# Kernel optimization log

Hardware: AMD Instinct MI355X
Metric: run time of the kernel (lower is better)

The kernel has to match this reference:

```python
import jax, jax.numpy as jnp
import numpy as np

V, N, F, H, E, C = 3, 20000, 256, 256, 160000, 32
NH = 8  # transformer heads


def setup_inputs() -> dict:
    key = jax.random.key(0)
    ks = jax.random.split(key, 24)
    r = lambda i, shape, s=0.05: jax.random.normal(ks[i], shape, jnp.float32) * s
    ri = lambda i, shape: jax.random.randint(ks[i], shape, 0, N)
    loop = jnp.arange(N)
    return {
        "x": r(0, (V, N, F), 1.0),
        "edge_src": ri(1, (V, E)),
        "edge_dst": ri(2, (V, E)),
        "g_src": jnp.concatenate([ri(3, (E,)), loop]),
        "g_dst": jnp.concatenate([ri(4, (E,)), loop]),
        "rand_w": r(5, (N, 1), 1.0),
        "gcn_W": r(6, (V, F, H)), "gcn_b": jnp.zeros((V, H)),
        "gat_W": r(7, (V, H, H)), "gat_asrc": r(8, (V, H)),
        "gat_adst": r(9, (V, H)), "gat_b": jnp.zeros((V, H)),
        "enc_Wqkv": r(10, (2, 3 * H, H)), "enc_bqkv": jnp.zeros((2, 3 * H)),
        "enc_Wo": r(11, (2, H, H)), "enc_bo": jnp.zeros((2, H)),
        "enc_W1": r(12, (2, 4 * H, H)), "enc_b1": jnp.zeros((2, 4 * H)),
        "enc_W2": r(13, (2, H, 4 * H)), "enc_b2": jnp.zeros((2, H)),
        "enc_ln1g": jnp.ones((2, H)), "enc_ln1b": jnp.zeros((2, H)),
        "enc_ln2g": jnp.ones((2, H)), "enc_ln2b": jnp.zeros((2, H)),
        "att_P": r(14, (2, H, 128)), "att_Pb": jnp.zeros((2, 128)),
        "att_q": r(15, (2, 128)),
        "mg_fc": r(16, (H, C)), "mg_al": r(17, (C,)), "mg_ar": r(18, (C,)),
        "mg_res": r(19, (H, C)),
    }


def _ln(x, g, b, eps=1e-5):
    m = x.mean(-1, keepdims=True)
    v = ((x - m) ** 2).mean(-1, keepdims=True)
    return (x - m) * jax.lax.rsqrt(v + eps) * g + b


def _gcn(x, src, dst, W, b):
    # PyG GCNConv: add self-loops, symmetric normalization, linear, scatter-sum
    n = x.shape[0]
    loop = jnp.arange(n)
    s = jnp.concatenate([src, loop])
    d = jnp.concatenate([dst, loop])
    h = x @ W  # [n, H]
    deg = jax.ops.segment_sum(jnp.ones_like(d, x.dtype), d, num_segments=n)
    dinv = jnp.where(deg > 0, jax.lax.rsqrt(deg), 0.0)
    norm = dinv[s] * dinv[d]  # [E+n]
    return jax.ops.segment_sum(h[s] * norm[:, None], d, num_segments=n) + b


def _edge_softmax(e, dst, n):
    m = jax.ops.segment_max(e, dst, num_segments=n)
    ee = jnp.exp(e - m[dst])
    z = jax.ops.segment_sum(ee, dst, num_segments=n)
    return ee / z[dst]


def _gat(x, src, dst, W, a_src, a_dst, b, slope=0.2):
    # PyG GATConv, heads=1, eval mode: add self-loops, attention softmax per dst
    n = x.shape[0]
    loop = jnp.arange(n)
    s = jnp.concatenate([src, loop])
    d = jnp.concatenate([dst, loop])
    h = x @ W
    e = jax.nn.leaky_relu((h @ a_src)[s] + (h @ a_dst)[d], slope)
    alpha = _edge_softmax(e, d, n)
    return jax.ops.segment_sum(h[s] * alpha[:, None], d, num_segments=n) + b


def _enc(x, Wqkv, bqkv, Wo, bo, W1, b1, W2, b2, g1, be1, g2, be2):
    # nn.TransformerEncoderLayer (post-norm, relu, eval): x is [S=V, B=N, H]
    S, B, Hd = x.shape
    dh = Hd // NH
    qkv = x @ Wqkv.T + bqkv
    q, k, v = jnp.split(qkv, 3, axis=-1)
    q = q.reshape(S, B, NH, dh)
    k = k.reshape(S, B, NH, dh)
    v = v.reshape(S, B, NH, dh)
    sc = jnp.einsum('sbhd,tbhd->bhst', q, k) * (1.0 / np.sqrt(dh))
    o = jnp.einsum('bhst,tbhd->sbhd', jax.nn.softmax(sc, axis=-1), v)
    o = o.reshape(S, B, Hd) @ Wo.T + bo
    h1 = _ln(x + o, g1, be1)
    ff = jax.nn.relu(h1 @ W1.T + b1) @ W2.T + b2
    return _ln(h1 + ff, g2, be2)


def reference(x, edge_src, edge_dst, g_src, g_dst, rand_w,
              gcn_W, gcn_b, gat_W, gat_asrc, gat_adst, gat_b,
              enc_Wqkv, enc_bqkv, enc_Wo, enc_bo, enc_W1, enc_b1, enc_W2, enc_b2,
              enc_ln1g, enc_ln1b, enc_ln2g, enc_ln2b,
              att_P, att_Pb, att_q, mg_fc, mg_al, mg_ar, mg_res):
    # multi-view GCN + relu
    emb1 = jax.nn.relu(jax.vmap(_gcn)(x, edge_src, edge_dst, gcn_W, gcn_b))
    a0 = _enc(emb1, enc_Wqkv[0], enc_bqkv[0], enc_Wo[0], enc_bo[0],
              enc_W1[0], enc_b1[0], enc_W2[0], enc_b2[0],
              enc_ln1g[0], enc_ln1b[0], enc_ln2g[0], enc_ln2b[0])
    # multi-view GAT + relu
    emb2 = jax.nn.relu(jax.vmap(_gat, in_axes=(0, 0, 0, 0, 0, 0, 0))(
        a0, edge_src, edge_dst, gat_W, gat_asrc, gat_adst, gat_b))
    a1 = _enc(emb2, enc_Wqkv[1], enc_bqkv[1], enc_Wo[1], enc_bo[1],
              enc_W1[1], enc_b1[1], enc_W2[1], enc_b2[1],
              enc_ln1g[1], enc_ln1b[1], enc_ln2g[1], enc_ln2b[1])
    # Attention over views (dim 0): tanh branch and relu branch, random blend
    w0 = jnp.tanh(a1 @ att_P[0] + att_Pb[0]) @ att_q[0][:, None]  # [V, N, 1]
    x1 = (jax.nn.softmax(w0, axis=0) * a1).sum(0)
    w1 = jax.nn.relu(a1 @ att_P[1] + att_Pb[1]) @ att_q[1][:, None]
    x2 = (jax.nn.softmax(w1, axis=0) * a1).sum(0)
    aw = jax.nn.softmax(rand_w, axis=0)  # [N, 1]
    g = aw * x1 + (1.0 - aw) * x2  # global_emb [N, H]
    # myGATConv (DGL-style, 1 head, residual linear, no bias/activation)
    f = g @ mg_fc  # [N, C]
    e = jax.nn.leaky_relu((f @ mg_al)[g_src] + (f @ mg_ar)[g_dst], 0.2)
    alpha = _edge_softmax(e, g_dst, N)
    rst = jax.ops.segment_sum(f[g_src] * alpha[:, None], g_dst, num_segments=N)
    rst = rst + g @ mg_res
    nrm = jnp.linalg.norm(rst, axis=1, keepdims=True)
    logits = rst / jnp.maximum(nrm, 1e-12)
    return (a0, a1, logits, g)
```

## Files before the change

### kernel.cpp

```cpp
#include <hip/hip_runtime.h>
#include <hip/hip_bf16.h>
#include <math.h>

namespace {
constexpr int kV  = 3;
constexpr int kN  = 20000;
constexpr int kF  = 256;
constexpr int kH  = 256;
constexpr int kE  = 160000;
constexpr int kC  = 32;
constexpr int kNH = 8;
constexpr int kSN = kV * kN;
constexpr int kE2 = kE + kN;
constexpr int kMP = 60160;

constexpr size_t OFF_T1   = 0;
constexpr size_t OFF_T2   = OFF_T1 + (size_t)kMP * 256;
constexpr size_t OFF_T3   = OFF_T2 + (size_t)kMP * 256;
constexpr size_t OFF_BIGB = OFF_T3 + (size_t)kMP * 256;
constexpr size_t OFF_SB   = OFF_BIGB + (size_t)kMP * 512;
constexpr size_t OFF_AB   = OFF_SB + (size_t)kMP * 128;
constexpr size_t OFF_WB   = OFF_AB + (size_t)kMP * 128;
constexpr size_t OFF_GWB  = OFF_WB + 786432;
constexpr size_t OFF_PB   = OFF_GWB + 196608;
constexpr size_t OFF_DEG  = OFF_PB + 32768;
constexpr size_t OFF_EL   = OFF_DEG + (size_t)kV * kN;
constexpr size_t OFF_ER   = OFF_EL  + (size_t)kV * kN;
constexpr size_t OFF_W0   = OFF_ER  + (size_t)kV * kN;
constexpr size_t OFF_W1   = OFF_W0  + (size_t)kV * kN;
constexpr size_t OFF_FB   = OFF_W1  + (size_t)kV * kN;
constexpr size_t OFF_R2   = OFF_FB  + (size_t)kN * kC;
constexpr size_t OFF_RST  = OFF_R2  + (size_t)kN * kC;
constexpr size_t OFF_EL2  = OFF_RST + (size_t)kN * kC;
constexpr size_t OFF_ER2  = OFF_EL2 + kN;
constexpr size_t OFF_ST   = OFF_ER2 + kN;
constexpr size_t OFF_INT  = OFF_ST + 4;
constexpr size_t ICNT  = 0;
constexpr size_t ICNT2 = ICNT  + (size_t)kV * kN;
constexpr size_t IOFF  = ICNT2 + kN;
constexpr size_t IOFF2 = IOFF  + (size_t)kV * kN;
constexpr size_t ICUR  = IOFF2 + kN;
constexpr size_t ICUR2 = ICUR  + (size_t)kV * kN;
constexpr size_t ICSR  = ICUR2 + kN;
constexpr size_t ICSR2 = ICSR  + (size_t)kV * kE;
}

typedef __attribute__((ext_vector_type(4))) float f32x4;
typedef __attribute__((ext_vector_type(8))) __bf16 bf16x8;

__device__ __forceinline__ float lrelu(float x) { return x > 0.f ? x : 0.2f * x; }
__device__ __forceinline__ unsigned short f2b(float f) {
    unsigned u = __float_as_uint(f);
    return (unsigned short)((u + 0x7FFFu + ((u >> 16) & 1u)) >> 16);
}
__device__ __forceinline__ float b2f(unsigned short h) {
    return __uint_as_float((unsigned)h << 16);
}
__device__ __forceinline__ float fast_tanh(float x) {
    float xc = fminf(fmaxf(x, -15.f), 15.f);
    float e = __expf(2.0f * xc);
    return (e - 1.0f) / (e + 1.0f);
}


__global__ void cvt_k(const float* __restrict__ in, unsigned short* __restrict__ out, int n4) {
    int i = blockIdx.x * 256 + threadIdx.x;
    if (i >= n4) return;
    float4 v = reinterpret_cast<const float4*>(in)[i];
    ushort4 o;
    o.x = f2b(v.x); o.y = f2b(v.y); o.z = f2b(v.z); o.w = f2b(v.w);
    reinterpret_cast<ushort4*>(out)[i] = o;
}

__global__ void tcvt_k(const float* __restrict__ in, unsigned short* __restrict__ out,
                       int K, int N, int total) {
    int gid = blockIdx.x * 256 + threadIdx.x;
    if (gid >= total) return;
    int per = K * N;
    int v = gid / per, r = gid - v * per;
    int n = r / K, k = r - n * K;
    out[gid] = f2b(in[(size_t)v * per + (size_t)k * N + n]);
}

template <int ACT, bool WF32, bool WB16>
__global__ __launch_bounds__(256, 4) void mgemm_k(const unsigned short* __restrict__ A,
                                                  const unsigned short* __restrict__ W,
                                                  const float* __restrict__ bias,
                                                  float* __restrict__ Cf,
                                                  unsigned short* __restrict__ Cb,
                                                  int M, int N, int K,
                                                  long zA, long zW, long zC) {
    static_assert(WF32 != WB16, "exactly one output path");
    __shared__ __align__(16) unsigned short shbuf[16384];

    const int tid  = threadIdx.x;
    const int lane = tid & 63;

    const int gx = gridDim.x;
    const int nwg = gx * gridDim.y;
    const int orig = blockIdx.y * gx + blockIdx.x;
    const int q = nwg >> 3, rr = nwg & 7;
    const int xcd = orig & 7, pos = orig >> 3;
    const int nid = (xcd < rr ? xcd * (q + 1) : rr * (q + 1) + (xcd - rr) * q) + pos;
    const int bm = (nid / gx) * 128, bn = (nid % gx) * 128;

    A += (size_t)blockIdx.z * zA;
    W += (size_t)blockIdx.z * zW;
    const size_t zrow = (size_t)blockIdx.z * zC;

    const int wv = tid >> 6;
    const int wm = (wv >> 1) * 64, wn = (wv & 1) * 64;
    const int fr = lane & 15;

    const int r0 = tid >> 2;
    const int xorv = (r0 >> 1) & 3;
// ... 45 lines not shown
        for (int mi = 0; mi < 4; ++mi)
            av[mi] = *reinterpret_cast<const bf16x8*>(As + (wm + mi * 16 + fr) * 32 + slr);
#pragma unroll
        for (int ni = 0; ni < 4; ++ni)
            bv[ni] = *reinterpret_cast<const bf16x8*>(Ws + (wn + ni * 16 + fr) * 32 + slr);
#pragma unroll
        for (int mi = 0; mi < 4; ++mi)
#pragma unroll
            for (int ni = 0; ni < 4; ++ni)
                acc[mi][ni] = __builtin_amdgcn_mfma_f32_16x16x32_bf16(av[mi], bv[ni], acc[mi][ni], 0, 0, 0);
        __syncthreads();
        cur ^= 1;
    }

    const int crow = (lane >> 4) * 4;
    const int ccol = lane & 15;

    if (WB16) {
#pragma unroll
        for (int mi = 0; mi < 4; ++mi)
#pragma unroll
            for (int r = 0; r < 4; ++r) {
                const int row = wm + mi * 16 + crow + r;
#pragma unroll
                for (int ni = 0; ni < 4; ++ni) {
                    const int col = wn + ni * 16 + ccol;
                    float v = acc[mi][ni][r];
                    if (bias) v += bias[bn + col];
                    if (ACT == 1) v = fmaxf(v, 0.f);
                    if (ACT == 2) v = fast_tanh(v);
                    if (ACT == 3) v = (bn + col < 128) ? fast_tanh(v) : fmaxf(v, 0.f);
                    shbuf[row * 128 + col] = f2b(v);
                }
            }
        __syncthreads();
#pragma unroll
        for (int it = 0; it < 8; ++it) {
            const int fl = it * 2048 + tid * 8;
            const int row = fl >> 7, col = fl & 127;
            const int grow = bm + row;
            if (grow < M) {
                uint4 d = *reinterpret_cast<const uint4*>(shbuf + row * 128 + col);
                *reinterpret_cast<uint4*>(Cb + (zrow + grow) * (size_t)N + bn + col) = d;
            }
        }
    } else {
        float* epf = reinterpret_cast<float*>(shbuf);
#pragma unroll
        for (int half = 0; half < 2; ++half) {
            if ((wm >> 6) == half) {
#pragma unroll
                for (int mi = 0; mi < 4; ++mi)
#pragma unroll
                    for (int r = 0; r < 4; ++r) {
                        const int row = mi * 16 + crow + r;
#pragma unroll
                        for (int ni = 0; ni < 4; ++ni) {
                            const int col = wn + ni * 16 + ccol;
                            float v = acc[mi][ni][r];
                            if (bias) v += bias[bn + col];
                            if (ACT == 1) v = fmaxf(v, 0.f);
                            if (ACT == 2) v = fast_tanh(v);
                            if (ACT == 3) v = (bn + col < 128) ? fast_tanh(v) : fmaxf(v, 0.f);
                            epf[row * 128 + col] = v;
                        }
                    }
            }
            __syncthreads();
#pragma unroll
            for (int it = 0; it < 8; ++it) {
                const int fl = it * 1024 + tid * 4;
                const int row = fl >> 7, col = fl & 127;
                const int grow = bm + half * 64 + row;
                if (grow < M) {
                    float4 d = *reinterpret_cast<const float4*>(epf + row * 128 + col);
                    *reinterpret_cast<float4*>(Cf + (zrow + grow) * (size_t)N + bn + col) = d;
                }
            }
            __syncthreads();
        }
    }
}

template <int ACT>
__global__ __launch_bounds__(256) void gemm_k(const float* __restrict__ A,
                                              const float* __restrict__ B,
                                              const float* __restrict__ bias,
                                              float* __restrict__ Cmat,
                                              int M, int Nn, int K) {
    __shared__ float As[16][64];
    __shared__ float Bs[16][68];
    const int tid  = threadIdx.x;
    const int bm   = blockIdx.y * 64;
    const int bn   = blockIdx.x * 64;
    const int tx   = tid & 15, ty = tid >> 4;
    const int arow = tid >> 2;
    const int acol = (tid & 3) << 2;
    const int brow = tid >> 4;
    const int bcol = (tid & 15) << 2;
    const int gm   = bm + arow;
    float acc[4][4] = {{0.f,0.f,0.f,0.f},{0.f,0.f,0.f,0.f},{0.f,0.f,0.f,0.f},{0.f,0.f,0.f,0.f}};

    for (int k0 = 0; k0 < K; k0 += 16) {
        float4 av = make_float4(0.f, 0.f, 0.f, 0.f);
        if (gm < M) av = *reinterpret_cast<const float4*>(A + (size_t)gm * K + (k0 + acol));
        As[acol + 0][arow] = av.x;
        As[acol + 1][arow] = av.y;
        As[acol + 2][arow] = av.z;
        As[acol + 3][arow] = av.w;

        const int gn = bn + bcol;
        const float* Brow = B + (size_t)(k0 + brow) * Nn;
        float4 bv;
        if (gn + 3 < Nn) {
            bv = *reinterpret_cast<const float4*>(Brow + gn);
        } else {
            bv.x = (gn + 0 < Nn) ? Brow[gn + 0] : 0.f;
            bv.y = (gn + 1 < Nn) ? Brow[gn + 1] : 0.f;
            bv.z = (gn + 2 < Nn) ? Brow[gn + 2] : 0.f;
            bv.w = (gn + 3 < Nn) ? Brow[gn + 3] : 0.f;
        }
        *reinterpret_cast<float4*>(&Bs[brow][bcol]) = bv;
        __syncthreads();

#pragma unroll
        for (int k = 0; k < 16; ++k) {
            float4 a4 = *reinterpret_cast<const float4*>(&As[k][ty << 2]);
            float4 b4 = *reinterpret_cast<const float4*>(&Bs[k][tx << 2]);
            acc[0][0] += a4.x * b4.x; acc[0][1] += a4.x * b4.y; acc[0][2] += a4.x * b4.z; acc[0][3] += a4.x * b4.w;
            acc[1][0] += a4.y * b4.x; acc[1][1] += a4.y * b4.y; acc[1][2] += a4.y * b4.z; acc[1][3] += a4.y * b4.w;
            acc[2][0] += a4.z * b4.x; acc[2][1] += a4.z * b4.y; acc[2][2] += a4.z * b4.z; acc[2][3] += a4.z * b4.w;
            acc[3][0] += a4.w * b4.x; acc[3][1] += a4.w * b4.y; acc[3][2] += a4.w * b4.z; acc[3][3] += a4.w * b4.w;
        }
        __syncthreads();
    }

#pragma unroll
    for (int i = 0; i < 4; ++i) {
        int m = bm + (ty << 2) + i;
        if (m >= M) continue;
#pragma unroll
        for (int j = 0; j < 4; ++j) {
            int n = bn + (tx << 2) + j;
            if (n >= Nn) continue;
            float v = acc[i][j];
            if (bias) v += bias[n];
            if (ACT == 1) v = fmaxf(v, 0.f);
            if (ACT == 2) v = fast_tanh(v);
            Cmat[(size_t)m * Nn + n] = v;
        }
    }
}

template <bool WF32>
__global__ __launch_bounds__(256) void ln_add_k(const unsigned short* __restrict__ x,
                                                const unsigned short* __restrict__ y,
                                                const float* __restrict__ g, const float* __restrict__ b,
                                                float* __restrict__ outf, unsigned short* __restrict__ outb,
                                                int rows) {
    int r = blockIdx.x * 4 + (threadIdx.x >> 6);
    if (r >= rows) return;
    int lane = threadIdx.x & 63;
    size_t base = (size_t)r * 256 + lane * 4;
    ushort4 xu = *reinterpret_cast<const ushort4*>(x + base);
    ushort4 yu = *reinterpret_cast<const ushort4*>(y + base);
    float4 t;
    t.x = b2f(xu.x) + b2f(yu.x); t.y = b2f(xu.y) + b2f(yu.y);
    t.z = b2f(xu.z) + b2f(yu.z); t.w = b2f(xu.w) + b2f(yu.w);
    float s = t.x + t.y + t.z + t.w;
#pragma unroll
    for (int off = 32; off > 0; off >>= 1) s += __shfl_xor(s, off, 64);
    float mean = s * (1.0f / 256.0f);
    float4 d;
    d.x = t.x - mean; d.y = t.y - mean; d.z = t.z - mean; d.w = t.w - mean;
    float s2 = d.x * d.x + d.y * d.y + d.z * d.z + d.w * d.w;
#pragma unroll
    for (int off = 32; off > 0; off >>= 1) s2 += __shfl_xor(s2, off, 64);
    float rs = rsqrtf(s2 * (1.0f / 256.0f) + 1e-5f);
    float4 gv = *reinterpret_cast<const float4*>(g + lane * 4);
    float4 bv = *reinterpret_cast<const float4*>(b + lane * 4);
    float4 o;
    o.x = d.x * rs * gv.x + bv.x;
    o.y = d.y * rs * gv.y + bv.y;
    o.z = d.z * rs * gv.z + bv.z;
    o.w = d.w * rs * gv.w + bv.w;
    if (WF32) *reinterpret_cast<float4*>(outf + base) = o;
    ushort4 ob;
    ob.x = f2b(o.x); ob.y = f2b(o.y); ob.z = f2b(o.z); ob.w = f2b(o.w);
    *reinterpret_cast<ushort4*>(outb + base) = ob;
}

__global__ void rowdot2_k(const float* __restrict__ A, const float* __restrict__ v1,
                          const float* __restrict__ v2, float* __restrict__ o1,
                          float* __restrict__ o2, int rows, int K, int rowsPerVec, int vecStride) {
    int r = blockIdx.x;
    if (r >= rows) return;
    int lane = threadIdx.x;
    const float* base = A + (size_t)r * K;
    int vo = (r / rowsPerVec) * vecStride;
    float s1 = 0.f, s2 = 0.f;
    for (int c = lane; c < K; c += 64) {
        float a = base[c];
        s1 += a * v1[vo + c];
        if (v2) s2 += a * v2[vo + c];
    }
#pragma unroll
    for (int off = 32; off > 0; off >>= 1) {
        s1 += __shfl_xor(s1, off, 64);
        s2 += __shfl_xor(s2, off, 64);
    }
    if (lane == 0) { o1[r] = s1; if (o2) o2[r] = s2; }
}

__global__ __launch_bounds__(256) void attdot_k(const unsigned short* __restrict__ A, const float* __restrict__ q,
                                                float* __restrict__ o1, float* __restrict__ o2, int rows) {
    int r = blockIdx.x * 4 + (threadIdx.x >> 6);
    if (r >= rows) return;
    int lane = threadIdx.x & 63;
    const unsigned short* row = A + (size_t)r * 256;
    ushort2 va = *reinterpret_cast<const ushort2*>(row + lane * 2);
    ushort2 vb = *reinterpret_cast<const ushort2*>(row + 128 + lane * 2);
    float2 qa = *reinterpret_cast<const float2*>(q + lane * 2);
    float2 qb = *reinterpret_cast<const float2*>(q + 128 + lane * 2);
    float s1 = b2f(va.x) * qa.x + b2f(va.y) * qa.y;
    float s2 = b2f(vb.x) * qb.x + b2f(vb.y) * qb.y;
#pragma unroll
    for (int off = 32; off > 0; off >>= 1) {
        s1 += __shfl_xor(s1, off, 64);
        s2 += __shfl_xor(s2, off, 64);
    }
    if (lane == 0) { o1[r] = s1; o2[r] = s2; }
}

__global__ void rowdot2b_k(const unsigned short* __restrict__ A, const float* __restrict__ v1,
                           const float* __restrict__ v2, float* __restrict__ o1,
                           float* __restrict__ o2, int rows, int K, int rowsPerVec, int vecStride) {
    int r = blockIdx.x;
    if (r >= rows) return;
    int lane = threadIdx.x;
    const unsigned short* base = A + (size_t)r * K;
    int vo = (r / rowsPerVec) * vecStride;
    float s1 = 0.f, s2 = 0.f;
    for (int c = lane * 4; c < K; c += 256) {
        ushort4 a4 = *reinterpret_cast<const ushort4*>(base + c);
        float4 w1 = *reinterpret_cast<const float4*>(v1 + vo + c);
        float4 w2 = *reinterpret_cast<const float4*>(v2 + vo + c);
        s1 += b2f(a4.x) * w1.x + b2f(a4.y) * w1.y + b2f(a4.z) * w1.z + b2f(a4.w) * w1.w;
        s2 += b2f(a4.x) * w2.x + b2f(a4.y) * w2.y + b2f(a4.z) * w2.z + b2f(a4.w) * w2.w;
    }
#pragma unroll
    for (int off = 32; off > 0; off >>= 1) {
        s1 += __shfl_xor(s1, off, 64);
        s2 += __shfl_xor(s2, off, 64);
    }
    if (lane == 0) { o1[r] = s1; o2[r] = s2; }
}


__global__ void count_k(const int* __restrict__ dst, int* __restrict__ cnt, int nE, int nN, int total) {
    int gid = blockIdx.x * 256 + threadIdx.x;
    if (gid >= total) return;
    int v = gid / nE;
    atomicAdd(&cnt[(size_t)v * nN + dst[gid]], 1);
}

__global__ __launch_bounds__(1024) void scan_k(const int* __restrict__ cnt, int* __restrict__ offs,
                                               int* __restrict__ cursor, int nN) {
    int v = blockIdx.x;
    const int* c = cnt + (size_t)v * nN;
    int* o  = offs + (size_t)v * nN;
    int* cu = cursor + (size_t)v * nN;
    int tid = threadIdx.x;
    int chunk = (nN + 1023) >> 10;
    int lo = tid * chunk;
    int hi = lo + chunk < nN ? lo + chunk : nN;
    int s = 0;
    for (int i = lo; i < hi; ++i) s += c[i];
    int lane = tid & 63, wid = tid >> 6;
    int x = s;
#pragma unroll
    for (int off = 1; off < 64; off <<= 1) {
        int y = __shfl_up(x, off, 64);
        if (lane >= off) x += y;
    }
    __shared__ int wsum[16];
    if (lane == 63) wsum[wid] = x;
    __syncthreads();
    if (tid == 0) {
        int a = 0;
        for (int w = 0; w < 16; ++w) { int t = wsum[w]; wsum[w] = a; a += t; }
    }
    __syncthreads();
    int base = x - s + wsum[wid];
    for (int i = lo; i < hi; ++i) { o[i] = base; cu[i] = base; base += c[i]; }
}

__global__ void fill_csr_k(const int* __restrict__ src, const int* __restrict__ dst,
                           int* __restrict__ cursor, int* __restrict__ csr,
                           int nE, int nN, int total) {
    int gid = blockIdx.x * 256 + threadIdx.x;
    if (gid >= total) return;
    int v = gid / nE;
    int pos = atomicAdd(&cursor[(size_t)v * nN + dst[gid]], 1);
    csr[(size_t)v * nE + pos] = src[gid];
}

__global__ void dinv_k(const int* __restrict__ cnt, float* __restrict__ dinv, int n) {
    int gid = blockIdx.x * 256 + threadIdx.x;
    if (gid < n) dinv[gid] = rsqrtf((float)cnt[gid] + 1.0f);
}


__global__ __launch_bounds__(256) void gcn_gather_k(const int* __restrict__ csr, const int* __restrict__ offs,
                                                    const int* __restrict__ cnt, const float* __restrict__ dinv,
                                                    const unsigned short* __restrict__ h, const float* __restrict__ b,
                                                    unsigned short* __restrict__ outb) {
    int nd = blockIdx.x * 4 + (threadIdx.x >> 6);
    if (nd >= kV * kN) return;
    int v  = nd / kN;
    int lane = threadIdx.x & 63;
    int c4 = lane * 4;
    const int* base = csr + (size_t)v * kE;
    int o0 = offs[nd], n = cnt[nd];
    float dd = dinv[nd];
    const float* dv = dinv + (size_t)v * kN;
    const unsigned short* hb = h + (size_t)v * kN * kH;

    ushort4 hs = *reinterpret_cast<const ushort4*>(h + (size_t)nd * kH + c4);
    float wts = dd * dd;
    float4 acc;
    acc.x = b2f(hs.x) * wts; acc.y = b2f(hs.y) * wts;
// ... 45 lines not shown
    float m = eself;
    for (int i = 0; i < n; ++i) m = fmaxf(m, lrelu(elv[base[o0 + i]] + erd));

    float es = __expf(eself - m);
    float z = es;
    ushort4 hs = *reinterpret_cast<const ushort4*>(h + (size_t)nd * kH + c4);
    float4 acc;
    acc.x = b2f(hs.x) * es; acc.y = b2f(hs.y) * es;
    acc.z = b2f(hs.z) * es; acc.w = b2f(hs.w) * es;
    int i = 0;
    for (; i + 2 <= n; i += 2) {
        int s0 = base[o0 + i], s1 = base[o0 + i + 1];
        float e0 = __expf(lrelu(elv[s0] + erd) - m);
        float e1 = __expf(lrelu(elv[s1] + erd) - m);
        z += e0 + e1;
        ushort4 h0 = *reinterpret_cast<const ushort4*>(hb + (size_t)s0 * kH + c4);
        ushort4 h1 = *reinterpret_cast<const ushort4*>(hb + (size_t)s1 * kH + c4);
        acc.x += b2f(h0.x) * e0 + b2f(h1.x) * e1;
        acc.y += b2f(h0.y) * e0 + b2f(h1.y) * e1;
        acc.z += b2f(h0.z) * e0 + b2f(h1.z) * e1;
        acc.w += b2f(h0.w) * e0 + b2f(h1.w) * e1;
    }
    if (i < n) {
        int s0 = base[o0 + i];
        float e0 = __expf(lrelu(elv[s0] + erd) - m);
        z += e0;
        ushort4 h0 = *reinterpret_cast<const ushort4*>(hb + (size_t)s0 * kH + c4);
        acc.x += b2f(h0.x) * e0; acc.y += b2f(h0.y) * e0;
        acc.z += b2f(h0.z) * e0; acc.w += b2f(h0.w) * e0;
    }
    float iz = 1.0f / z;
    float4 bb = *reinterpret_cast<const float4*>(b + (size_t)v * kH + c4);
    ushort4 ob;
    ob.x = f2b(fmaxf(acc.x * iz + bb.x, 0.f));
    ob.y = f2b(fmaxf(acc.y * iz + bb.y, 0.f));
    ob.z = f2b(fmaxf(acc.z * iz + bb.z, 0.f));
    ob.w = f2b(fmaxf(acc.w * iz + bb.w, 0.f));
    *reinterpret_cast<ushort4*>(outb + (size_t)nd * kH + c4) = ob;
}


__global__ __launch_bounds__(256) void mha3_k(const unsigned short* __restrict__ qkv, unsigned short* __restrict__ o) {
    int grp = blockIdx.x * 32 + (threadIdx.x >> 3);
    int l8 = threadIdx.x & 7;
    if (grp >= kN * kNH) return;
    int b = grp / kNH, h = grp - b * kNH;
    float4 q[3], k[3], vv[3];
#pragma unroll
    for (int s = 0; s < 3; ++s) {
        size_t base = ((size_t)s * kN + b) * 768 + h * 32 + l8 * 4;
        ushort4 qu = *reinterpret_cast<const ushort4*>(qkv + base);
        ushort4 ku = *reinterpret_cast<const ushort4*>(qkv + base + 256);
        ushort4 vu = *reinterpret_cast<const ushort4*>(qkv + base + 512);
        q[s].x = b2f(qu.x); q[s].y = b2f(qu.y); q[s].z = b2f(qu.z); q[s].w = b2f(qu.w);
        k[s].x = b2f(ku.x); k[s].y = b2f(ku.y); k[s].z = b2f(ku.z); k[s].w = b2f(ku.w);
        vv[s].x = b2f(vu.x); vv[s].y = b2f(vu.y); vv[s].z = b2f(vu.z); vv[s].w = b2f(vu.w);
    }
    float sc[3][3];
#pragma unroll
    for (int s = 0; s < 3; ++s)
#pragma unroll
        for (int t = 0; t < 3; ++t) {
            float d = q[s].x * k[t].x + q[s].y * k[t].y + q[s].z * k[t].z + q[s].w * k[t].w;
            d += __shfl_xor(d, 1, 64);
            d += __shfl_xor(d, 2, 64);
            d += __shfl_xor(d, 4, 64);
            sc[s][t] = d * 0.17677669529663687f;
        }
#pragma unroll
    for (int s = 0; s < 3; ++s) {
        float m = fmaxf(sc[s][0], fmaxf(sc[s][1], sc[s][2]));
        float e0 = __expf(sc[s][0] - m), e1 = __expf(sc[s][1] - m), e2 = __expf(sc[s][2] - m);
        float iz = 1.0f / (e0 + e1 + e2);
        ushort4 ob;
        ob.x = f2b((e0 * vv[0].x + e1 * vv[1].x + e2 * vv[2].x) * iz);
        ob.y = f2b((e0 * vv[0].y + e1 * vv[1].y + e2 * vv[2].y) * iz);
        ob.z = f2b((e0 * vv[0].z + e1 * vv[1].z + e2 * vv[2].z) * iz);
        ob.w = f2b((e0 * vv[0].w + e1 * vv[1].w + e2 * vv[2].w) * iz);
        *reinterpret_cast<ushort4*>(o + ((size_t)s * kN + b) * kH + h * 32 + l8 * 4) = ob;
    }
}


__global__ void view_comb_k(const unsigned short* __restrict__ a1b, const float* __restrict__ w0,
                            const float* __restrict__ w1, float* __restrict__ x1,
                            float* __restrict__ x2) {
    int gid = blockIdx.x * 256 + threadIdx.x;
    if (gid >= kN * 64) return;
    int n = gid >> 6;
    int c4 = (gid & 63) << 2;
    float u0 = w0[n], u1 = w0[kN + n], u2 = w0[2 * kN + n];
    float m = fmaxf(u0, fmaxf(u1, u2));
    float e0 = __expf(u0 - m), e1 = __expf(u1 - m), e2 = __expf(u2 - m);
    float iz = 1.f / (e0 + e1 + e2);
    float p0 = e0 * iz, p1 = e1 * iz, p2 = e2 * iz;
    float q0 = w1[n], q1 = w1[kN + n], q2 = w1[2 * kN + n];
    float mq = fmaxf(q0, fmaxf(q1, q2));
    float f0 = __expf(q0 - mq), f1 = __expf(q1 - mq), f2 = __expf(q2 - mq);
    float izq = 1.f / (f0 + f1 + f2);
    float r0 = f0 * izq, r1 = f1 * izq, r2 = f2 * izq;
    ushort4 U0 = *reinterpret_cast<const ushort4*>(a1b + ((size_t)0 * kN + n) * 256 + c4);
    ushort4 U1 = *reinterpret_cast<const ushort4*>(a1b + ((size_t)1 * kN + n) * 256 + c4);
    ushort4 U2 = *reinterpret_cast<const ushort4*>(a1b + ((size_t)2 * kN + n) * 256 + c4);
    float4 A0 = make_float4(b2f(U0.x), b2f(U0.y), b2f(U0.z), b2f(U0.w));
    float4 A1 = make_float4(b2f(U1.x), b2f(U1.y), b2f(U1.z), b2f(U1.w));
    float4 A2 = make_float4(b2f(U2.x), b2f(U2.y), b2f(U2.z), b2f(U2.w));
    float4 o1, o2;
    o1.x = p0 * A0.x + p1 * A1.x + p2 * A2.x;  o2.x = r0 * A0.x + r1 * A1.x + r2 * A2.x;
    o1.y = p0 * A0.y + p1 * A1.y + p2 * A2.y;  o2.y = r0 * A0.y + r1 * A1.y + r2 * A2.y;
    o1.z = p0 * A0.z + p1 * A1.z + p2 * A2.z;  o2.z = r0 * A0.z + r1 * A1.z + r2 * A2.z;
    o1.w = p0 * A0.w + p1 * A1.w + p2 * A2.w;  o2.w = r0 * A0.w + r1 * A1.w + r2 * A2.w;
    *reinterpret_cast<float4*>(x1 + (size_t)n * 256 + c4) = o1;
    *reinterpret_cast<float4*>(x2 + (size_t)n * 256 + c4) = o2;
}

__global__ __launch_bounds__(1024) void randsm_k(const float* __restrict__ rw, float* __restrict__ stats) {
    __shared__ float sm[16];
    __shared__ float ss[16];
    int tid = threadIdx.x;
    float m = -1e30f;
    for (int i = tid; i < kN; i += 1024) m = fmaxf(m, rw[i]);
#pragma unroll
    for (int off = 32; off > 0; off >>= 1) m = fmaxf(m, __shfl_xor(m, off, 64));
    if ((tid & 63) == 0) sm[tid >> 6] = m;
    __syncthreads();
    if (tid == 0) {
        float mm = sm[0];
        for (int i = 1; i < 16; ++i) mm = fmaxf(mm, sm[i]);
        sm[0] = mm;
    }
    __syncthreads();
    float mx = sm[0];
    float s = 0.f;
    for (int i = tid; i < kN; i += 1024) s += __expf(rw[i] - mx);
#pragma unroll
    for (int off = 32; off > 0; off >>= 1) s += __shfl_xor(s, off, 64);
    if ((tid & 63) == 0) ss[tid >> 6] = s;
    __syncthreads();
    if (tid == 0) {
        float z = 0.f;
        for (int i = 0; i < 16; ++i) z += ss[i];
        stats[0] = mx;
        stats[1] = z;
    }
}

__global__ void blend_k(const float* __restrict__ x1, const float* __restrict__ x2,
                        const float* __restrict__ rw, const float* __restrict__ stats,
                        float* __restrict__ g) {
    int gid = blockIdx.x * 256 + threadIdx.x;
    if (gid >= kN * 64) return;
    int n = gid >> 6;
    int c4 = (gid & 63) << 2;
    float aw = __expf(rw[n] - stats[0]) / stats[1];
    float4 v1 = *reinterpret_cast<const float4*>(x1 + (size_t)n * 256 + c4);
    float4 v2 = *reinterpret_cast<const float4*>(x2 + (size_t)n * 256 + c4);
    float4 o;
    o.x = aw * v1.x + (1.f - aw) * v2.x;
    o.y = aw * v1.y + (1.f - aw) * v2.y;
    o.z = aw * v1.z + (1.f - aw) * v2.z;
    o.w = aw * v1.w + (1.f - aw) * v2.w;
    *reinterpret_cast<float4*>(g + (size_t)n * 256 + c4) = o;
}


__global__ __launch_bounds__(256) void mygat_gather_k(const int* __restrict__ csr, const int* __restrict__ offs,
                                                      const int* __restrict__ cnt, const float* __restrict__ el,
                                                      const float* __restrict__ er, const float* __restrict__ f,
                                                      float* __restrict__ rst) {
    int node = blockIdx.x * 8 + (threadIdx.x >> 5);
    int c = threadIdx.x & 31;
    if (node >= kN) return;
    int o0 = offs[node], n = cnt[node];
    float erd = er[node];
    float m = -1e30f;
    for (int i = 0; i < n; ++i) {
        int s = csr[o0 + i];
        m = fmaxf(m, lrelu(el[s] + erd));
    }
    float z = 0.f, acc = 0.f;
    for (int i = 0; i < n; ++i) {
        int s = csr[o0 + i];
        float e = __expf(lrelu(el[s] + erd) - m);
        z += e;
        acc += f[(size_t)s * kC + c] * e;
    }
    rst[(size_t)node * kC + c] = acc / z;
}

__global__ void final_k(const float* __restrict__ rst, const float* __restrict__ r2,
                        float* __restrict__ logits) {
    int n = blockIdx.x * 256 + threadIdx.x;
    if (n >= kN) return;
    float vals[kC];
    float ssum = 0.f;
#pragma unroll
    for (int c = 0; c < kC; ++c) {
        vals[c] = rst[(size_t)n * kC + c] + r2[(size_t)n * kC + c];
        ssum += vals[c] * vals[c];
    }
    float inv = 1.0f / fmaxf(sqrtf(ssum), 1e-12f);
#pragma unroll
    for (int c = 0; c < kC; ++c) logits[(size_t)n * kC + c] = vals[c] * inv;
}


static void run_encoder(unsigned short* xinB, float* outp, unsigned short* outB, float* ws, int e,
                        const float* bqkv, const float* bo, const float* b1, const float* b2,
                        const float* g1, const float* be1, const float* g2, const float* be2,
                        hipStream_t stream) {
    unsigned short* T2B  = (unsigned short*)(ws + OFF_T2);
    unsigned short* BIGB = (unsigned short*)(ws + OFF_BIGB);
    unsigned short* OB   = BIGB + (size_t)kMP * 768;
    unsigned short* WB   = (unsigned short*)(ws + OFF_WB);
    const unsigned short* WQ = WB + (size_t)e * 196608;
    const unsigned short* WO = WB + 393216 + (size_t)e * 65536;
    const unsigned short* W1 = WB + 524288 + (size_t)e * 262144;
    const unsigned short* W2 = WB + 1048576 + (size_t)e * 262144;
    dim3 blk(256);

    mgemm_k<0, false, true><<<dim3(6, 469, 1), blk, 0, stream>>>(
        xinB, WQ, bqkv, nullptr, BIGB, kSN, 768, 256, 0, 0, 0);
    mha3_k<<<dim3((kN * kNH) / 32), blk, 0, stream>>>(BIGB, OB);
    mgemm_k<0, false, true><<<dim3(2, 469, 1), blk, 0, stream>>>(
        OB, WO, bo, nullptr, T2B, kSN, 256, 256, 0, 0, 0);
    ln_add_k<false><<<dim3(kSN / 4), blk, 0, stream>>>(xinB, T2B, g1, be1, nullptr, xinB, kSN);
    mgemm_k<1, false, true><<<dim3(8, 469, 1), blk, 0, stream>>>(
        xinB, W1, b1, nullptr, BIGB, kSN, 1024, 256, 0, 0, 0);
    mgemm_k<0, false, true><<<dim3(2, 469, 1), blk, 0, stream>>>(
        BIGB, W2, b2, nullptr, T2B, kSN, 256, 1024, 0, 0, 0);
    ln_add_k<true><<<dim3(kSN / 4), blk, 0, stream>>>(xinB, T2B, g2, be2, outp, outB, kSN);
}

extern "C" void kernel_launch(void* const* d_in, const int* in_sizes, int n_in,
                              void* d_out, int out_size, void* d_ws, size_t ws_size,
                              hipStream_t stream) {
    (void)in_sizes; (void)n_in; (void)out_size; (void)ws_size;

    const float* x      = (const float*)d_in[0];
    const int*   e_src  = (const int*)d_in[1];
    const int*   e_dst  = (const int*)d_in[2];
    const int*   gsrc   = (const int*)d_in[3];
    const int*   gdst   = (const int*)d_in[4];
    const float* rand_w = (const float*)d_in[5];
    const float* gcn_W  = (const float*)d_in[6];
    const float* gcn_b  = (const float*)d_in[7];
    const float* gat_W  = (const float*)d_in[8];
    const float* gat_as = (const float*)d_in[9];
    const float* gat_ad = (const float*)d_in[10];
    const float* gat_b  = (const float*)d_in[11];
    const float* Wqkv   = (const float*)d_in[12];
    const float* bqkv   = (const float*)d_in[13];
    const float* Wo     = (const float*)d_in[14];
    const float* bo     = (const float*)d_in[15];
    const float* W1     = (const float*)d_in[16];
    const float* b1     = (const float*)d_in[17];
    const float* W2     = (const float*)d_in[18];
    const float* b2     = (const float*)d_in[19];
    const float* ln1g   = (const float*)d_in[20];
    const float* ln1b   = (const float*)d_in[21];
    const float* ln2g   = (const float*)d_in[22];
    const float* ln2b   = (const float*)d_in[23];
    const float* att_P  = (const float*)d_in[24];
    const float* att_Pb = (const float*)d_in[25];
    const float* att_q  = (const float*)d_in[26];
    const float* mg_fc  = (const float*)d_in[27];
    const float* mg_al  = (const float*)d_in[28];
    const float* mg_ar  = (const float*)d_in[29];
    const float* mg_res = (const float*)d_in[30];

    float* ws  = (float*)d_ws;
    float* T3  = ws + OFF_T3;
    float* DNV = ws + OFF_DEG;
    float* EL  = ws + OFF_EL;
    float* ER  = ws + OFF_ER;
    float* W0b = ws + OFF_W0;
    float* W1b = ws + OFF_W1;
    float* FB  = ws + OFF_FB;
    float* R2  = ws + OFF_R2;
    float* RST = ws + OFF_RST;
    float* EL2 = ws + OFF_EL2;
    float* ER2 = ws + OFF_ER2;
    float* ST  = ws + OFF_ST;

    unsigned short* T2B  = (unsigned short*)(ws + OFF_T2);
    unsigned short* BIGB = (unsigned short*)(ws + OFF_BIGB);
    unsigned short* HB   = BIGB;
    unsigned short* SB   = (unsigned short*)(ws + OFF_SB);
    unsigned short* AB   = (unsigned short*)(ws + OFF_AB);
    unsigned short* WB   = (unsigned short*)(ws + OFF_WB);
    unsigned short* GWB  = (unsigned short*)(ws + OFF_GWB);
    unsigned short* PB   = (unsigned short*)(ws + OFF_PB);

    int* ib    = (int*)(ws + OFF_INT);
    int* CNT   = ib + ICNT;
    int* CNT2  = ib + ICNT2;
    int* OFFS  = ib + IOFF;
    int* OFFS2 = ib + IOFF2;
    int* CUR   = ib + ICUR;
    int* CUR2  = ib + ICUR2;
    int* CSR   = ib + ICSR;
    int* CSR2  = ib + ICSR2;

    float* outp   = (float*)d_out;
    float* a0     = outp;
    float* a1     = outp + (size_t)kSN * kH;
    float* logits = outp + 2 * (size_t)kSN * kH;
    float* gemb   = outp + 2 * (size_t)kSN * kH + (size_t)kN * kC;

    dim3 blk(256);

    hipMemsetAsync(SB + (size_t)kSN * 256, 0, (size_t)(kMP - kSN) * 256 * sizeof(unsigned short), stream);
    hipMemsetAsync(AB + (size_t)kSN * 256, 0, (size_t)(kMP - kSN) * 256 * sizeof(unsigned short), stream);
    hipMemsetAsync(BIGB + (size_t)kSN * 1024, 0, (size_t)(kMP - kSN) * 1024 * sizeof(unsigned short), stream);

    hipMemsetAsync(CNT, 0, (size_t)(kV * kN + kN) * sizeof(int), stream);
    count_k<<<dim3((kV * kE + 255) / 256), blk, 0, stream>>>(e_dst, CNT, kE, kN, kV * kE);
    count_k<<<dim3((kE2 + 255) / 256), blk, 0, stream>>>(gdst, CNT2, kE2, kN, kE2);
    scan_k<<<dim3(kV), dim3(1024), 0, stream>>>(CNT, OFFS, CUR, kN);
    scan_k<<<dim3(1), dim3(1024), 0, stream>>>(CNT2, OFFS2, CUR2, kN);
    fill_csr_k<<<dim3((kV * kE + 255) / 256), blk, 0, stream>>>(e_src, e_dst, CUR, CSR, kE, kN, kV * kE);
    fill_csr_k<<<dim3((kE2 + 255) / 256), blk, 0, stream>>>(gsrc, gdst, CUR2, CSR2, kE2, kN, kE2);
    dinv_k<<<dim3((kV * kN + 255) / 256), blk, 0, stream>>>(CNT, DNV, kV * kN);

    cvt_k<<<dim3((393216 / 4 + 255) / 256), blk, 0, stream>>>(Wqkv, WB, 393216 / 4);
    cvt_k<<<dim3((131072 / 4 + 255) / 256), blk, 0, stream>>>(Wo, WB + 393216, 131072 / 4);
    cvt_k<<<dim3((524288 / 4 + 255) / 256), blk, 0, stream>>>(W1, WB + 524288, 524288 / 4);
    cvt_k<<<dim3((524288 / 4 + 255) / 256), blk, 0, stream>>>(W2, WB + 1048576, 524288 / 4);
    tcvt_k<<<dim3((3 * 65536 + 255) / 256), blk, 0, stream>>>(gcn_W, GWB, 256, 256, 3 * 65536);
    tcvt_k<<<dim3((3 * 65536 + 255) / 256), blk, 0, stream>>>(gat_W, GWB + 3 * 65536, 256, 256, 3 * 65536);
    tcvt_k<<<dim3((2 * 32768 + 255) / 256), blk, 0, stream>>>(att_P, PB, 256, 128, 2 * 32768);
    cvt_k<<<dim3((kSN * 256 / 4 + 255) / 256), blk, 0, stream>>>(x, AB, kSN * 256 / 4);

    mgemm_k<0, false, true><<<dim3(2, 157, 3), blk, 0, stream>>>(
        AB, GWB, nullptr, nullptr, HB, kN, 256, 256, (long)kN * 256, 65536, kN);
    gcn_gather_k<<<dim3(kSN / 4), blk, 0, stream>>>(CSR, OFFS, CNT, DNV, HB, gcn_b, SB);

    run_encoder(SB, a0, AB, ws, 0, bqkv, bo, b1, b2, ln1g, ln1b, ln2g, ln2b, stream);

    mgemm_k<0, false, true><<<dim3(2, 157, 3), blk, 0, stream>>>(
        AB, GWB + 3 * 65536, nullptr, nullptr, HB, kN, 256, 256, (long)kN * 256, 65536, kN);
    rowdot2b_k<<<dim3(kSN), dim3(64), 0, stream>>>(HB, gat_as, gat_ad, EL, ER, kSN, 256, kN, kH);
    gat_gather_k<<<dim3(kSN / 4), blk, 0, stream>>>(CSR, OFFS, CNT, EL, ER, HB, gat_b, SB);

    run_encoder(SB, a1, AB, ws, 1, bqkv + 768, bo + 256, b1 + 1024, b2 + 256,
                ln1g + 256, ln1b + 256, ln2g + 256, ln2b + 256, stream);

    mgemm_k<3, false, true><<<dim3(2, 469, 1), blk, 0, stream>>>(
        AB, PB, att_Pb, nullptr, T2B, kSN, 256, 256, 0, 0, 0);
    attdot_k<<<dim3(kSN / 4), blk, 0, stream>>>(T2B, att_q, W0b, W1b, kSN);
    float* X1 = T3;
    float* X2 = T3 + (size_t)kN * kH;
    view_comb_k<<<dim3((kN * 64 + 255) / 256), blk, 0, stream>>>(AB, W0b, W1b, X1, X2);
    randsm_k<<<dim3(1), dim3(1024), 0, stream>>>(rand_w, ST);
    blend_k<<<dim3((kN * 64 + 255) / 256), blk, 0, stream>>>(X1, X2, rand_w, ST, gemb);

    gemm_k<0><<<dim3(1, (kN + 63) / 64), blk, 0, stream>>>(gemb, mg_fc, (const float*)nullptr, FB, kN, kC, 256);
    rowdot2_k<<<dim3(kN), dim3(64), 0, stream>>>(FB, mg_al, mg_ar, EL2, ER2, kN, kC, kN, 0);
    mygat_gather_k<<<dim3((kN + 7) / 8), blk, 0, stream>>>(CSR2, OFFS2, CNT2, EL2, ER2, FB, RST);
    gemm_k<0><<<dim3(1, (kN + 63) / 64), blk, 0, stream>>>(gemb, mg_res, (const float*)nullptr, R2, kN, kC, 256);
    final_k<<<dim3((kN + 255) / 256), blk, 0, stream>>>(RST, R2, logits);
}
```

Before: 979.5 us.

## Fuse view attention with blend and run final projections on bf16 matrix GEMM

Merges view_comb_k and blend_k into a single kernel that folds the random blend weight into the per-view softmax coefficients, so the two fp32 N×256 intermediates are never written or re-read. The global embedding is also stored as bf16. The two small fp32 GEMMs (mg_fc and mg_res) become one bf16 matrix GEMM with a concatenated, zero-padded 128-wide weight, and a lighter mgdot kernel reads the attention dots from that output. This adds bf16 rounding to the myGAT path and pads the output to 128 columns, which wastes some compute.

```diff
diff --git a/kernel.cpp b/kernel.cpp
--- a/kernel.cpp
+++ b/kernel.cpp
@@ -13,8 +13,12 @@
 constexpr int kSN = kV * kN;
 constexpr int kE2 = kE + kN;
 constexpr int kMP = 60160;
+constexpr int kNP = 20224;
 
 constexpr size_t OFF_T1   = 0;
+constexpr size_t OFF_GB   = OFF_T1;
+constexpr size_t OFF_FB1  = OFF_T1 + 2600000;
+constexpr size_t OFF_WMG  = OFF_T1 + 5200000;
 constexpr size_t OFF_T2   = OFF_T1 + (size_t)kMP * 256;
 constexpr size_t OFF_T3   = OFF_T2 + (size_t)kMP * 256;
 constexpr size_t OFF_BIGB = OFF_T3 + (size_t)kMP * 256;
@@ -28,9 +32,7 @@
 constexpr size_t OFF_ER   = OFF_EL  + (size_t)kV * kN;
 constexpr size_t OFF_W0   = OFF_ER  + (size_t)kV * kN;
 constexpr size_t OFF_W1   = OFF_W0  + (size_t)kV * kN;
-constexpr size_t OFF_FB   = OFF_W1  + (size_t)kV * kN;
-constexpr size_t OFF_R2   = OFF_FB  + (size_t)kN * kC;
-constexpr size_t OFF_RST  = OFF_R2  + (size_t)kN * kC;
+constexpr size_t OFF_RST  = OFF_W1  + (size_t)kV * kN;
 constexpr size_t OFF_EL2  = OFF_RST + (size_t)kN * kC;
 constexpr size_t OFF_ER2  = OFF_EL2 + kN;
 constexpr size_t OFF_ST   = OFF_ER2 + kN;
@@ -242,76 +244,6 @@
     }
 }
 
-template <int ACT>
-__global__ __launch_bounds__(256) void gemm_k(const float* __restrict__ A,
-                                              const float* __restrict__ B,
-                                              const float* __restrict__ bias,
-                                              float* __restrict__ Cmat,
-                                              int M, int Nn, int K) {
-    __shared__ float As[16][64];
-    __shared__ float Bs[16][68];
-    const int tid  = threadIdx.x;
-    const int bm   = blockIdx.y * 64;
-    const int bn   = blockIdx.x * 64;
-    const int tx   = tid & 15, ty = tid >> 4;
-    const int arow = tid >> 2;
-    const int acol = (tid & 3) << 2;
-    const int brow = tid >> 4;
-    const int bcol = (tid & 15) << 2;
-    const int gm   = bm + arow;
-    float acc[4][4] = {{0.f,0.f,0.f,0.f},{0.f,0.f,0.f,0.f},{0.f,0.f,0.f,0.f},{0.f,0.f,0.f,0.f}};
-
-    for (int k0 = 0; k0 < K; k0 += 16) {
-        float4 av = make_float4(0.f, 0.f, 0.f, 0.f);
-        if (gm < M) av = *reinterpret_cast<const float4*>(A + (size_t)gm * K + (k0 + acol));
-        As[acol + 0][arow] = av.x;
-        As[acol + 1][arow] = av.y;
-        As[acol + 2][arow] = av.z;
-        As[acol + 3][arow] = av.w;
-
-        const int gn = bn + bcol;
-        const float* Brow = B + (size_t)(k0 + brow) * Nn;
-        float4 bv;
-        if (gn + 3 < Nn) {
-            bv = *reinterpret_cast<const float4*>(Brow + gn);
-        } else {
-            bv.x = (gn + 0 < Nn) ? Brow[gn + 0] : 0.f;
-            bv.y = (gn + 1 < Nn) ? Brow[gn + 1] : 0.f;
-            bv.z = (gn + 2 < Nn) ? Brow[gn + 2] : 0.f;
-            bv.w = (gn + 3 < Nn) ? Brow[gn + 3] : 0.f;
-        }
-        *reinterpret_cast<float4*>(&Bs[brow][bcol]) = bv;
-        __syncthreads();
-
-#pragma unroll
-        for (int k = 0; k < 16; ++k) {
-            float4 a4 = *reinterpret_cast<const float4*>(&As[k][ty << 2]);
-            float4 b4 = *reinterpret_cast<const float4*>(&Bs[k][tx << 2]);
-            acc[0][0] += a4.x * b4.x; acc[0][1] += a4.x * b4.y; acc[0][2] += a4.x * b4.z; acc[0][3] += a4.x * b4.w;
-            acc[1][0] += a4.y * b4.x; acc[1][1] += a4.y * b4.y; acc[1][2] += a4.y * b4.z; acc[1][3] += a4.y * b4.w;
-            acc[2][0] += a4.z * b4.x; acc[2][1] += a4.z * b4.y; acc[2][2] += a4.z * b4.z; acc[2][3] += a4.z * b4.w;
-            acc[3][0] += a4.w * b4.x; acc[3][1] += a4.w * b4.y; acc[3][2] += a4.w * b4.z; acc[3][3] += a4.w * b4.w;
-        }
-        __syncthreads();
-    }
-
-#pragma unroll
-    for (int i = 0; i < 4; ++i) {
-        int m = bm + (ty << 2) + i;
-        if (m >= M) continue;
-#pragma unroll
-        for (int j = 0; j < 4; ++j) {
-            int n = bn + (tx << 2) + j;
-            if (n >= Nn) continue;
-            float v = acc[i][j];
-            if (bias) v += bias[n];
-            if (ACT == 1) v = fmaxf(v, 0.f);
-            if (ACT == 2) v = fast_tanh(v);
-            Cmat[(size_t)m * Nn + n] = v;
-        }
-    }
-}
-
 template <bool WF32>
 __global__ __launch_bounds__(256) void ln_add_k(const unsigned short* __restrict__ x,
                                                 const unsigned short* __restrict__ y,
@@ -350,28 +282,6 @@
     *reinterpret_cast<ushort4*>(outb + base) = ob;
 }
 
-__global__ void rowdot2_k(const float* __restrict__ A, const float* __restrict__ v1,
-                          const float* __restrict__ v2, float* __restrict__ o1,
-                          float* __restrict__ o2, int rows, int K, int rowsPerVec, int vecStride) {
-    int r = blockIdx.x;
-    if (r >= rows) return;
-    int lane = threadIdx.x;
-    const float* base = A + (size_t)r * K;
-    int vo = (r / rowsPerVec) * vecStride;
-    float s1 = 0.f, s2 = 0.f;
-    for (int c = lane; c < K; c += 64) {
-        float a = base[c];
-        s1 += a * v1[vo + c];
-        if (v2) s2 += a * v2[vo + c];
-    }
-#pragma unroll
-    for (int off = 32; off > 0; off >>= 1) {
-        s1 += __shfl_xor(s1, off, 64);
-        s2 += __shfl_xor(s2, off, 64);
-    }
-    if (lane == 0) { o1[r] = s1; if (o2) o2[r] = s2; }
-}
-
 __global__ __launch_bounds__(256) void attdot_k(const unsigned short* __restrict__ A, const float* __restrict__ q,
                                                 float* __restrict__ o1, float* __restrict__ o2, int rows) {
     int r = blockIdx.x * 4 + (threadIdx.x >> 6);
@@ -407,6 +317,26 @@
         float4 w2 = *reinterpret_cast<const float4*>(v2 + vo + c);
         s1 += b2f(a4.x) * w1.x + b2f(a4.y) * w1.y + b2f(a4.z) * w1.z + b2f(a4.w) * w1.w;
         s2 += b2f(a4.x) * w2.x + b2f(a4.y) * w2.y + b2f(a4.z) * w2.z + b2f(a4.w) * w2.w;
+    }
+#pragma unroll
+    for (int off = 32; off > 0; off >>= 1) {
+        s1 += __shfl_xor(s1, off, 64);
+        s2 += __shfl_xor(s2, off, 64);
+    }
+    if (lane == 0) { o1[r] = s1; o2[r] = s2; }
+}
+
+__global__ __launch_bounds__(256) void mgdot_k(const float* __restrict__ F, const float* __restrict__ al,
+                                               const float* __restrict__ ar, float* __restrict__ o1,
+                                               float* __restrict__ o2, int rows) {
+    int r = blockIdx.x * 4 + (threadIdx.x >> 6);
+    if (r >= rows) return;
+    int lane = threadIdx.x & 63;
+    float s1 = 0.f, s2 = 0.f;
+    if (lane < 32) {
+        float a = F[(size_t)r * 128 + lane];
+        s1 = a * al[lane];
+        s2 = a * ar[lane];
     }
 #pragma unroll
     for (int off = 32; off > 0; off >>= 1) {
@@ -618,9 +548,10 @@
 }
 
 
-__global__ void view_comb_k(const unsigned short* __restrict__ a1b, const float* __restrict__ w0,
-                            const float* __restrict__ w1, float* __restrict__ x1,
-                            float* __restrict__ x2) {
+__global__ void view_blend_k(const unsigned short* __restrict__ a1b, const float* __restrict__ w0,
+                             const float* __restrict__ w1, const float* __restrict__ rw,
+                             const float* __restrict__ stats, float* __restrict__ gout,
+                             unsigned short* __restrict__ gb) {
     int gid = blockIdx.x * 256 + threadIdx.x;
     if (gid >= kN * 64) return;
     int n = gid >> 6;
@@ -635,19 +566,22 @@
     float f0 = __expf(q0 - mq), f1 = __expf(q1 - mq), f2 = __expf(q2 - mq);
     float izq = 1.f / (f0 + f1 + f2);
     float r0 = f0 * izq, r1 = f1 * izq, r2 = f2 * izq;
+    float aw = __expf(rw[n] - stats[0]) / stats[1];
+    float b0 = aw * p0 + (1.f - aw) * r0;
+    float b1v = aw * p1 + (1.f - aw) * r1;
+    float b2v = aw * p2 + (1.f - aw) * r2;
     ushort4 U0 = *reinterpret_cast<const ushort4*>(a1b + ((size_t)0 * kN + n) * 256 + c4);
     ushort4 U1 = *reinterpret_cast<const ushort4*>(a1b + ((size_t)1 * kN + n) * 256 + c4);
     ushort4 U2 = *reinterpret_cast<const ushort4*>(a1b + ((size_t)2 * kN + n) * 256 + c4);
-    float4 A0 = make_float4(b2f(U0.x), b2f(U0.y), b2f(U0.z), b2f(U0.w));
-    float4 A1 = make_float4(b2f(U1.x), b2f(U1.y), b2f(U1.z), b2f(U1.w));
-    float4 A2 = make_float4(b2f(U2.x), b2f(U2.y), b2f(U2.z), b2f(U2.w));
-    float4 o1, o2;
-    o1.x = p0 * A0.x + p1 * A1.x + p2 * A2.x;  o2.x = r0 * A0.x + r1 * A1.x + r2 * A2.x;
-    o1.y = p0 * A0.y + p1 * A1.y + p2 * A2.y;  o2.y = r0 * A0.y + r1 * A1.y + r2 * A2.y;
-    o1.z = p0 * A0.z + p1 * A1.z + p2 * A2.z;  o2.z = r0 * A0.z + r1 * A1.z + r2 * A2.z;
-    o1.w = p0 * A0.w + p1 * A1.w + p2 * A2.w;  o2.w = r0 * A0.w + r1 * A1.w + r2 * A2.w;
-    *reinterpret_cast<float4*>(x1 + (size_t)n * 256 + c4) = o1;
-    *reinterpret_cast<float4*>(x2 + (size_t)n * 256 + c4) = o2;
+    float4 o;
+    o.x = b0 * b2f(U0.x) + b1v * b2f(U1.x) + b2v * b2f(U2.x);
+    o.y = b0 * b2f(U0.y) + b1v * b2f(U1.y) + b2v * b2f(U2.y);
+    o.z = b0 * b2f(U0.z) + b1v * b2f(U1.z) + b2v * b2f(U2.z);
+    o.w = b0 * b2f(U0.w) + b1v * b2f(U1.w) + b2v * b2f(U2.w);
+    *reinterpret_cast<float4*>(gout + (size_t)n * 256 + c4) = o;
+    ushort4 ob;
+    ob.x = f2b(o.x); ob.y = f2b(o.y); ob.z = f2b(o.z); ob.w = f2b(o.w);
+    *reinterpret_cast<ushort4*>(gb + (size_t)n * 256 + c4) = ob;
 }
 
 __global__ __launch_bounds__(1024) void randsm_k(const float* __restrict__ rw, float* __restrict__ stats) {
@@ -679,24 +613,6 @@
         stats[0] = mx;
         stats[1] = z;
     }
-}
-
-__global__ void blend_k(const float* __restrict__ x1, const float* __restrict__ x2,
-                        const float* __restrict__ rw, const float* __restrict__ stats,
-                        float* __restrict__ g) {
-    int gid = blockIdx.x * 256 + threadIdx.x;
-    if (gid >= kN * 64) return;
-    int n = gid >> 6;
-    int c4 = (gid & 63) << 2;
-    float aw = __expf(rw[n] - stats[0]) / stats[1];
-    float4 v1 = *reinterpret_cast<const float4*>(x1 + (size_t)n * 256 + c4);
-    float4 v2 = *reinterpret_cast<const float4*>(x2 + (size_t)n * 256 + c4);
-    float4 o;
-    o.x = aw * v1.x + (1.f - aw) * v2.x;
-    o.y = aw * v1.y + (1.f - aw) * v2.y;
-    o.z = aw * v1.z + (1.f - aw) * v2.z;
-    o.w = aw * v1.w + (1.f - aw) * v2.w;
-    *reinterpret_cast<float4*>(g + (size_t)n * 256 + c4) = o;
 }
 
 
@@ -719,12 +635,12 @@
         int s = csr[o0 + i];
         float e = __expf(lrelu(el[s] + erd) - m);
         z += e;
-        acc += f[(size_t)s * kC + c] * e;
+        acc += f[(size_t)s * 128 + c] * e;
     }
     rst[(size_t)node * kC + c] = acc / z;
 }
 
-__global__ void final_k(const float* __restrict__ rst, const float* __restrict__ r2,
+__global__ void final_k(const float* __restrict__ rst, const float* __restrict__ F,
                         float* __restrict__ logits) {
     int n = blockIdx.x * 256 + threadIdx.x;
     if (n >= kN) return;
@@ -732,7 +648,7 @@
     float ssum = 0.f;
 #pragma unroll
     for (int c = 0; c < kC; ++c) {
-        vals[c] = rst[(size_t)n * kC + c] + r2[(size_t)n * kC + c];
+        vals[c] = rst[(size_t)n * kC + c] + F[(size_t)n * 128 + 32 + c];
         ssum += vals[c] * vals[c];
     }
     float inv = 1.0f / fmaxf(sqrtf(ssum), 1e-12f);
@@ -806,19 +722,19 @@
     const float* mg_res = (const float*)d_in[30];
 
     float* ws  = (float*)d_ws;
-    float* T3  = ws + OFF_T3;
     float* DNV = ws + OFF_DEG;
     float* EL  = ws + OFF_EL;
     float* ER  = ws + OFF_ER;
     float* W0b = ws + OFF_W0;
     float* W1b = ws + OFF_W1;
-    float* FB  = ws + OFF_FB;
-    float* R2  = ws + OFF_R2;
     float* RST = ws + OFF_RST;
     float* EL2 = ws + OFF_EL2;
     float* ER2 = ws + OFF_ER2;
     float* ST  = ws + OFF_ST;
-
+    float* FB128 = ws + OFF_FB1;
+
+    unsigned short* GB   = (unsigned short*)(ws + OFF_GB);
+    unsigned short* WMG  = (unsigned short*)(ws + OFF_WMG);
     unsigned short* T2B  = (unsigned short*)(ws + OFF_T2);
     unsigned short* BIGB = (unsigned short*)(ws + OFF_BIGB);
     unsigned short* HB   = BIGB;
@@ -849,6 +765,8 @@
     hipMemsetAsync(SB + (size_t)kSN * 256, 0, (size_t)(kMP - kSN) * 256 * sizeof(unsigned short), stream);
     hipMemsetAsync(AB + (size_t)kSN * 256, 0, (size_t)(kMP - kSN) * 256 * sizeof(unsigned short), stream);
     hipMemsetAsync(BIGB + (size_t)kSN * 1024, 0, (size_t)(kMP - kSN) * 1024 * sizeof(unsigned short), stream);
+    hipMemsetAsync(GB + (size_t)kN * 256, 0, (size_t)(kNP - kN) * 256 * sizeof(unsigned short), stream);
+    hipMemsetAsync(WMG, 0, 128 * 256 * sizeof(unsigned short), stream);
 
     hipMemsetAsync(CNT, 0, (size_t)(kV * kN + kN) * sizeof(int), stream);
     count_k<<<dim3((kV * kE + 255) / 256), blk, 0, stream>>>(e_dst, CNT, kE, kN, kV * kE);
@@ -866,6 +784,8 @@
     tcvt_k<<<dim3((3 * 65536 + 255) / 256), blk, 0, stream>>>(gcn_W, GWB, 256, 256, 3 * 65536);
     tcvt_k<<<dim3((3 * 65536 + 255) / 256), blk, 0, stream>>>(gat_W, GWB + 3 * 65536, 256, 256, 3 * 65536);
     tcvt_k<<<dim3((2 * 32768 + 255) / 256), blk, 0, stream>>>(att_P, PB, 256, 128, 2 * 32768);
+    tcvt_k<<<dim3((8192 + 255) / 256), blk, 0, stream>>>(mg_fc, WMG, 256, 32, 8192);
+    tcvt_k<<<dim3((8192 + 255) / 256), blk, 0, stream>>>(mg_res, WMG + 32 * 256, 256, 32, 8192);
     cvt_k<<<dim3((kSN * 256 / 4 + 255) / 256), blk, 0, stream>>>(x, AB, kSN * 256 / 4);
 
     mgemm_k<0, false, true><<<dim3(2, 157, 3), blk, 0, stream>>>(
@@ -885,15 +805,12 @@
     mgemm_k<3, false, true><<<dim3(2, 469, 1), blk, 0, stream>>>(
         AB, PB, att_Pb, nullptr, T2B, kSN, 256, 256, 0, 0, 0);
     attdot_k<<<dim3(kSN / 4), blk, 0, stream>>>(T2B, att_q, W0b, W1b, kSN);
-    float* X1 = T3;
-    float* X2 = T3 + (size_t)kN * kH;
-    view_comb_k<<<dim3((kN * 64 + 255) / 256), blk, 0, stream>>>(AB, W0b, W1b, X1, X2);
     randsm_k<<<dim3(1), dim3(1024), 0, stream>>>(rand_w, ST);
-    blend_k<<<dim3((kN * 64 + 255) / 256), blk, 0, stream>>>(X1, X2, rand_w, ST, gemb);
-
-    gemm_k<0><<<dim3(1, (kN + 63) / 64), blk, 0, stream>>>(gemb, mg_fc, (const float*)nullptr, FB, kN, kC, 256);
-    rowdot2_k<<<dim3(kN), dim3(64), 0, stream>>>(FB, mg_al, mg_ar, EL2, ER2, kN, kC, kN, 0);
-    mygat_gather_k<<<dim3((kN + 7) / 8), blk, 0, stream>>>(CSR2, OFFS2, CNT2, EL2, ER2, FB, RST);
-    gemm_k<0><<<dim3(1, (kN + 63) / 64), blk, 0, stream>>>(gemb, mg_res, (const float*)nullptr, R2, kN, kC, 256);
-    final_k<<<dim3((kN + 255) / 256), blk, 0, stream>>>(RST, R2, logits);
-}
+    view_blend_k<<<dim3((kN * 64 + 255) / 256), blk, 0, stream>>>(AB, W0b, W1b, rand_w, ST, gemb, GB);
+
+    mgemm_k<0, true, false><<<dim3(1, kNP / 128, 1), blk, 0, stream>>>(
+        GB, WMG, nullptr, FB128, nullptr, kN, 128, 256, 0, 0, 0);
+    mgdot_k<<<dim3((kN + 3) / 4), blk, 0, stream>>>(FB128, mg_al, mg_ar, EL2, ER2, kN);
+    mygat_gather_k<<<dim3((kN + 7) / 8), blk, 0, stream>>>(CSR2, OFFS2, CNT2, EL2, ER2, FB128, RST);
+    final_k<<<dim3((kN + 255) / 256), blk, 0, stream>>>(RST, FB128, logits);
+}
```

Measured after the change: 935.5 us (median of 2 runs). 4.5% less time.
